# Kernel tuning notes

Hardware: AMD Instinct MI355X
Metric: run time of the kernel (lower is better)

## Reference

```python
import jax, jax.numpy as jnp
import numpy as np

B, CW_DIM = 256, 8192
DIM_EMBED = 128
DICT_SIZE = 4096
DIM_CODES = CW_DIM // DIM_EMBED  # 64


def setup_inputs() -> dict:
    key = jax.random.key(0)
    k1, k2 = jax.random.split(key)
    x = jax.random.normal(k1, (B, CW_DIM), dtype=jnp.float32)
    dictionary = jax.random.normal(k2, (DIM_CODES, DICT_SIZE, DIM_EMBED), dtype=jnp.float32)
    return {"x": x, "dictionary": dictionary}


def reference(x, dictionary):
    """VQVAE.quantise (eval mode): pairwise sq-distance -> argmin -> gather + one-hot.

    x: [B, cw_dim], dictionary: [C, S, E] with cw_dim = C*E.
    Returns (cw_embed [B, C*E], one_hot_idx [B, C, S]).
    """
    Bb, D = x.shape
    C, S, E = dictionary.shape
    xr = x.reshape(Bb, C, E)                                   # [B, C, E]
    x_sq = jnp.sum(xr * xr, axis=-1, keepdims=True)            # [B, C, 1]
    d_sq = jnp.sum(dictionary * dictionary, axis=-1)           # [C, S]
    cross = jnp.einsum('bce,cse->bcs', xr, dictionary)         # [B, C, S] (GEMM)
    dist = x_sq + d_sq[None, :, :] - 2.0 * cross               # [B, C, S]
    idx = jnp.argmin(dist, axis=-1)                            # [B, C]
    # gather nearest codes: dictionary[c, idx[b,c]] -> [B, C, E]
    code_ids = jnp.arange(C)[None, :]                          # [1, C]
    cw_embed = dictionary[code_ids, idx]                       # [B, C, E]
    cw_embed = cw_embed.reshape(Bb, C * E)                     # [B, cw_dim]
    one_hot_idx = jax.nn.one_hot(idx, S, dtype=x.dtype)        # [B, C, S]
    return cw_embed, one_hot_idx
```

## Files before the change

kernel.cpp:

```cpp
#include <hip/hip_runtime.h>
#include <stdint.h>


#define B_SZ 256
#define C_SZ 64
#define E_SZ 128
#define S_SZ 4096
#define CW   8192
#define LDB  136

typedef __attribute__((ext_vector_type(4))) float    float4a;
typedef __attribute__((ext_vector_type(8))) _Float16 half8;

__device__ __forceinline__ void split8(float4a f0, float4a f1, half8& hi, half8& lo) {
    #pragma unroll
    for (int j = 0; j < 4; ++j) {
        _Float16 h0 = (_Float16)f0[j];
        hi[j]     = h0;
        lo[j]     = (_Float16)(f0[j] - (float)h0);
        _Float16 h1 = (_Float16)f1[j];
        hi[4 + j] = h1;
        lo[4 + j] = (_Float16)(f1[j] - (float)h1);
    }
}

__global__ __launch_bounds__(512, 2) void argmin_mfma(
    const float* __restrict__ x,
    const float* __restrict__ dict,
    int* __restrict__ idx_out,
    float* __restrict__ cw_out)
{
    __shared__ __attribute__((aligned(16))) _Float16 bh[2][128 * LDB];
    __shared__ __attribute__((aligned(16))) _Float16 bl[2][128 * LDB];
    __shared__ float4a dsqp[2][128];
    __shared__ int     fid[64];
    float* rv = reinterpret_cast<float*>(bh);
    int*   ri = reinterpret_cast<int*>(bl);

    const int tid   = threadIdx.x;
    const int lane  = tid & 63;
    const int quad  = lane >> 4;
    const int l15   = lane & 15;
    const int wid   = tid >> 6;
    const int mhalf = wid & 1;
    const int nquad = wid >> 1;
    const int c     = blockIdx.x & 63;
    const int btile = blockIdx.x >> 6;

    int m_attr[4], n_attr[4];
    {
        half8 ones, enc;
        #pragma unroll
        for (int j = 0; j < 8; ++j) { ones[j] = (_Float16)1.0f; enc[j] = (_Float16)(float)l15; }
        float4a z = {0.f, 0.f, 0.f, 0.f};
        float4a pr = __builtin_amdgcn_mfma_f32_16x16x32_f16(enc, ones, z, 0, 0, 0);
        float4a pc = __builtin_amdgcn_mfma_f32_16x16x32_f16(ones, enc, z, 0, 0, 0);
        #pragma unroll
        for (int r = 0; r < 4; ++r) {
            m_attr[r] = (int)(pr[r] * 0.03125f + 0.5f);
            n_attr[r] = (int)(pc[r] * 0.03125f + 0.5f);
        }
    }

    half8 ah[2][4], al[2][4];
    #pragma unroll
    for (int mi = 0; mi < 2; ++mi) {
        int b = btile * 64 + mhalf * 32 + mi * 16 + l15;
        const float* xr = x + (size_t)b * CW + c * E_SZ;
        #pragma unroll
        for (int kk = 0; kk < 4; ++kk) {
            float4a f0 = *reinterpret_cast<const float4a*>(xr + kk * 32 + quad * 8);
            float4a f1 = *reinterpret_cast<const float4a*>(xr + kk * 32 + quad * 8 + 4);
            split8(f0, f1, ah[mi][kk], al[mi][kk]);
        }
    }

    const int srow = tid >> 2;
    const int kq   = (tid & 3) * 32;
    const int q4   = tid & 3;
    const float* drow = dict + ((size_t)c * S_SZ + srow) * E_SZ + kq;

    float4a pf0[4], pf1[4];
    #pragma unroll
    for (int ck = 0; ck < 4; ++ck) {
        pf0[ck] = *reinterpret_cast<const float4a*>(drow + ck * 8);
        pf1[ck] = *reinterpret_cast<const float4a*>(drow + ck * 8 + 4);
    }
    {
        float dp = 0.f;
        #pragma unroll
        for (int ck = 0; ck < 4; ++ck) {
            half8 h, l;
            split8(pf0[ck], pf1[ck], h, l);
            #pragma unroll
            for (int j = 0; j < 4; ++j) {
                dp = fmaf(pf0[ck][j], pf0[ck][j], dp);
                dp = fmaf(pf1[ck][j], pf1[ck][j], dp);
            }
            *reinterpret_cast<half8*>(&bh[0][srow * LDB + kq + ck * 8]) = h;
            *reinterpret_cast<half8*>(&bl[0][srow * LDB + kq + ck * 8]) = l;
        }
        dsqp[0][srow][q4] = dp;
    }

    float bestv[8];
    int   besti[8];
    #pragma unroll
    for (int i = 0; i < 8; ++i) { bestv[i] = 3.4e38f; besti[i] = 0; }

    __syncthreads();

    int cur = 0;
    for (int it = 0; it < 32; ++it) {
        const int s0 = it * 128;

        if (it + 1 < 32) {
            const float* dr = drow + (size_t)(it + 1) * (128 * E_SZ);
            #pragma unroll
            for (int ck = 0; ck < 4; ++ck) {
                pf0[ck] = *reinterpret_cast<const float4a*>(dr + ck * 8);
                pf1[ck] = *reinterpret_cast<const float4a*>(dr + ck * 8 + 4);
            }
        }

        const _Float16* bhc = bh[cur];
        const _Float16* blc = bl[cur];
        float4a acc[2][2] = {{{0.f,0.f,0.f,0.f},{0.f,0.f,0.f,0.f}},
                             {{0.f,0.f,0.f,0.f},{0.f,0.f,0.f,0.f}}};
        #pragma unroll
        for (int kk = 0; kk < 4; ++kk) {
            half8 bhf[2], blf[2];
            #pragma unroll
            for (int ni = 0; ni < 2; ++ni) {
                const int sl = nquad * 32 + ni * 16 + l15;
                bhf[ni] = *reinterpret_cast<const half8*>(bhc + sl * LDB + kk * 32 + quad * 8);
                blf[ni] = *reinterpret_cast<const half8*>(blc + sl * LDB + kk * 32 + quad * 8);
            }
            #pragma unroll
            for (int mi = 0; mi < 2; ++mi)
                #pragma unroll
                for (int ni = 0; ni < 2; ++ni) {
                    acc[mi][ni] = __builtin_amdgcn_mfma_f32_16x16x32_f16(
                        ah[mi][kk], bhf[ni], acc[mi][ni], 0, 0, 0);
                    acc[mi][ni] = __builtin_amdgcn_mfma_f32_16x16x32_f16(
                        ah[mi][kk], blf[ni], acc[mi][ni], 0, 0, 0);
                    acc[mi][ni] = __builtin_amdgcn_mfma_f32_16x16x32_f16(
                        al[mi][kk], bhf[ni], acc[mi][ni], 0, 0, 0);
                }
        }

        #pragma unroll
        for (int ni = 0; ni < 2; ++ni)
            #pragma unroll
            for (int r = 0; r < 4; ++r) {
                const int sl = nquad * 32 + ni * 16 + n_attr[r];
                float4a q4v = dsqp[cur][sl];
                float dsq = (q4v[0] + q4v[1]) + (q4v[2] + q4v[3]);
                int sg = s0 + sl;
                #pragma unroll
                for (int mi = 0; mi < 2; ++mi) {
                    float dist = dsq - 2.0f * acc[mi][ni][r];
                    int slot = mi * 4 + r;
                    if (dist < bestv[slot]) { bestv[slot] = dist; besti[slot] = sg; }
                }
            }

        if (it + 1 < 32) {
            const int nb = cur ^ 1;
            float dp = 0.f;
            #pragma unroll
            for (int ck = 0; ck < 4; ++ck) {
                half8 h, l;
                split8(pf0[ck], pf1[ck], h, l);
                #pragma unroll
                for (int j = 0; j < 4; ++j) {
                    dp = fmaf(pf0[ck][j], pf0[ck][j], dp);
                    dp = fmaf(pf1[ck][j], pf1[ck][j], dp);
                }
                *reinterpret_cast<half8*>(&bh[nb][srow * LDB + kq + ck * 8]) = h;
                *reinterpret_cast<half8*>(&bl[nb][srow * LDB + kq + ck * 8]) = l;
            }
            dsqp[nb][srow][q4] = dp;
        }
        __syncthreads();
        cur ^= 1;
    }


    #pragma unroll
    for (int mi = 0; mi < 2; ++mi)
        #pragma unroll
        for (int r = 0; r < 4; ++r) {
            int row = mhalf * 32 + mi * 16 + m_attr[r];
            int col = nquad * 16 + n_attr[r];
            rv[row * 64 + col] = bestv[mi * 4 + r];
            ri[row * 64 + col] = besti[mi * 4 + r];
        }
    __syncthreads();

    if (tid < 64) {
        float bv = 3.4e38f; int bi = 0x7fffffff;
        for (int j = 0; j < 64; ++j) {
            float v = rv[tid * 64 + j];
            int   i = ri[tid * 64 + j];
            if (v < bv || (v == bv && i < bi)) { bv = v; bi = i; }
        }
        idx_out[(btile * 64 + tid) * C_SZ + c] = bi;
        fid[tid] = bi;
    }
    __syncthreads();

    for (int u = tid; u < 64 * 32; u += 512) {
        int row = u >> 5, ch = u & 31;
        int bi = fid[row];
        float4a v = *reinterpret_cast<const float4a*>(
            dict + ((size_t)c * S_SZ + bi) * E_SZ + ch * 4);
        *reinterpret_cast<float4a*>(
            cw_out + (size_t)(btile * 64 + row) * CW + c * E_SZ + ch * 4) = v;
    }
}

__global__ __launch_bounds__(256) void fill_onehot(
    const int* __restrict__ idx, float* __restrict__ oh)
{
    const int row = blockIdx.x;
    const int bi  = idx[row];
    float* base = oh + (size_t)row * S_SZ;
    const int t = threadIdx.x;
    #pragma unroll
    for (int j = 0; j < 4; ++j) {
        const int ch = j * 256 + t;
        float4a v = {0.f, 0.f, 0.f, 0.f};
        if ((bi >> 2) == ch) v[bi & 3] = 1.0f;
        __builtin_nontemporal_store(v, reinterpret_cast<float4a*>(base + (size_t)ch * 4));
    }
}

extern "C" void kernel_launch(void* const* d_in, const int* in_sizes, int n_in,
                              void* d_out, int out_size, void* d_ws, size_t ws_size,
                              hipStream_t stream) {
    const float* x    = (const float*)d_in[0];
    const float* dict = (const float*)d_in[1];
    float* out = (float*)d_out;
    int* idx = (int*)d_ws;
    float* oh = out + (size_t)B_SZ * CW;

    argmin_mfma<<<dim3(256), dim3(512), 0, stream>>>(x, dict, idx, out);
    fill_onehot<<<dim3(B_SZ * C_SZ), dim3(256), 0, stream>>>(idx, oh);
}
```

Baseline: 466.8 us.

## Fuse one-hot fill into argmin kernel, interleaving zero stores with the MFMA loop

Removes the separate one-hot kernel and its idx round-trip through workspace. Each block zero-fills its 64 rows of one-hot output with nontemporal stores spread across the 32 main-loop iterations, then writes the 1.0 after the argmin. The aim is to hide the 268MB write behind compute. It also raises wave priority around the MFMA section. The risk is that store traffic contends with the dictionary loads, and the ordering of the zero stores against the final 1.0 store relies on the block barrier.

```diff
diff --git a/kernel.cpp b/kernel.cpp
--- a/kernel.cpp
+++ b/kernel.cpp
@@ -27,8 +27,8 @@
 __global__ __launch_bounds__(512, 2) void argmin_mfma(
     const float* __restrict__ x,
     const float* __restrict__ dict,
-    int* __restrict__ idx_out,
-    float* __restrict__ cw_out)
+    float* __restrict__ cw_out,
+    float* __restrict__ oh)
 {
     __shared__ __attribute__((aligned(16))) _Float16 bh[2][128 * LDB];
     __shared__ __attribute__((aligned(16))) _Float16 bl[2][128 * LDB];
@@ -80,6 +80,9 @@
     const int q4   = tid & 3;
     const float* drow = dict + ((size_t)c * S_SZ + srow) * E_SZ + kq;
 
+    float* ohb = oh + ((size_t)(btile * 64) * C_SZ + c) * S_SZ;
+    const size_t oh_bstride = (size_t)C_SZ * S_SZ;
+
     float4a pf0[4], pf1[4];
     #pragma unroll
     for (int ck = 0; ck < 4; ++ck) {
@@ -121,12 +124,23 @@
                 pf0[ck] = *reinterpret_cast<const float4a*>(dr + ck * 8);
                 pf1[ck] = *reinterpret_cast<const float4a*>(dr + ck * 8 + 4);
             }
+        }
+
+        {
+            float4a zz = {0.f, 0.f, 0.f, 0.f};
+            float* z0 = ohb + (size_t)(it * 2) * oh_bstride;
+            float* z1 = z0 + oh_bstride;
+            __builtin_nontemporal_store(zz, reinterpret_cast<float4a*>(z0) + tid);
+            __builtin_nontemporal_store(zz, reinterpret_cast<float4a*>(z0) + 512 + tid);
+            __builtin_nontemporal_store(zz, reinterpret_cast<float4a*>(z1) + tid);
+            __builtin_nontemporal_store(zz, reinterpret_cast<float4a*>(z1) + 512 + tid);
         }
 
         const _Float16* bhc = bh[cur];
         const _Float16* blc = bl[cur];
         float4a acc[2][2] = {{{0.f,0.f,0.f,0.f},{0.f,0.f,0.f,0.f}},
                              {{0.f,0.f,0.f,0.f},{0.f,0.f,0.f,0.f}}};
+        __builtin_amdgcn_s_setprio(1);
         #pragma unroll
         for (int kk = 0; kk < 4; ++kk) {
             half8 bhf[2], blf[2];
@@ -148,6 +162,7 @@
                         al[mi][kk], bhf[ni], acc[mi][ni], 0, 0, 0);
                 }
         }
+        __builtin_amdgcn_s_setprio(0);
 
         #pragma unroll
         for (int ni = 0; ni < 2; ++ni)
@@ -205,8 +220,8 @@
             int   i = ri[tid * 64 + j];
             if (v < bv || (v == bv && i < bi)) { bv = v; bi = i; }
         }
-        idx_out[(btile * 64 + tid) * C_SZ + c] = bi;
         fid[tid] = bi;
+        ohb[(size_t)tid * oh_bstride + bi] = 1.0f;
     }
     __syncthreads();
 
@@ -220,31 +235,13 @@
     }
 }
 
-__global__ __launch_bounds__(256) void fill_onehot(
-    const int* __restrict__ idx, float* __restrict__ oh)
-{
-    const int row = blockIdx.x;
-    const int bi  = idx[row];
-    float* base = oh + (size_t)row * S_SZ;
-    const int t = threadIdx.x;
-    #pragma unroll
-    for (int j = 0; j < 4; ++j) {
-        const int ch = j * 256 + t;
-        float4a v = {0.f, 0.f, 0.f, 0.f};
-        if ((bi >> 2) == ch) v[bi & 3] = 1.0f;
-        __builtin_nontemporal_store(v, reinterpret_cast<float4a*>(base + (size_t)ch * 4));
-    }
-}
-
 extern "C" void kernel_launch(void* const* d_in, const int* in_sizes, int n_in,
                               void* d_out, int out_size, void* d_ws, size_t ws_size,
                               hipStream_t stream) {
     const float* x    = (const float*)d_in[0];
     const float* dict = (const float*)d_in[1];
     float* out = (float*)d_out;
-    int* idx = (int*)d_ws;
-    float* oh = out + (size_t)B_SZ * CW;
-
-    argmin_mfma<<<dim3(256), dim3(512), 0, stream>>>(x, dict, idx, out);
-    fill_onehot<<<dim3(B_SZ * C_SZ), dim3(256), 0, stream>>>(idx, oh);
+    float* oh  = out + (size_t)B_SZ * CW;
+
+    argmin_mfma<<<dim3(256), dim3(512), 0, stream>>>(x, dict, out, oh);
 }
```

Measured after the change: 462.5 us. About the same (-0.9%).
